# Optimization experiments

Hardware: AMD Instinct MI355X
Metric: run time of the kernel (lower is better)

Reference implementation:

```python
import jax, jax.numpy as jnp
import numpy as np
import math

N_HEAD = 16
STRIDE = 128
C = 8


def _sparse_causal_mask(q_len, k_len):
    # Mirrors LingLongAttention._sparse_causal_mask (static, host-side numpy).
    cols = np.arange(k_len)
    rows = np.arange(k_len)[:, None]
    strided = (cols % STRIDE) >= (STRIDE - C)          # last C cols of each stride block
    local = (cols[None, :] // STRIDE) == (rows // STRIDE)  # same stride block as query
    causal = cols[None, :] <= rows
    layout = (strided[None, :] | local) & causal       # [k_len, k_len]
    return jnp.asarray(layout[k_len - q_len:])         # [q_len, k_len]


def setup_inputs() -> dict:
    key = jax.random.key(0)
    k1, k2, k3 = jax.random.split(key, 3)
    B, S, E = 2, 2048, 1024
    return {
        "hidden_states": jax.random.normal(k1, (B, S, E), dtype=jnp.float32),
        "W_attn": jax.random.normal(k2, (E, 3 * E), dtype=jnp.float32) * 0.02,
        "b_attn": jnp.zeros((3 * E,), dtype=jnp.float32),
        "W_proj": jax.random.normal(k3, (E, E), dtype=jnp.float32) * 0.02,
        "b_proj": jnp.zeros((E,), dtype=jnp.float32),
    }


def reference(hidden_states, W_attn, b_attn, W_proj, b_proj):
    B, S, E = hidden_states.shape
    H = N_HEAD
    D = E // H
    # Conv1D: x @ W + b, then split into q,k,v
    qkv = hidden_states @ W_attn + b_attn                 # [B,S,3E]
    q, k, v = jnp.split(qkv, 3, axis=-1)
    split = lambda t: t.reshape(B, S, H, D).transpose(0, 2, 1, 3)  # [B,H,S,D]
    q, k, v = split(q), split(k), split(v)
    scale = jnp.asarray(1.0 / math.sqrt(D), dtype=q.dtype)
    scores = jnp.einsum("bhqd,bhkd->bhqk", q, k) * scale  # [B,H,S,S]
    mask = _sparse_causal_mask(S, S)[None, None]          # [1,1,S,S]
    mask_value = jnp.asarray(jnp.finfo(scores.dtype).min, dtype=scores.dtype)
    scores = jnp.where(mask, scores, mask_value)
    attn = jax.nn.softmax(scores, axis=-1)
    out = jnp.einsum("bhqk,bhkd->bhqd", attn, v)          # [B,H,S,D]
    out = out.transpose(0, 2, 1, 3).reshape(B, S, E)      # merge heads
    return out @ W_proj + b_proj
```

## Files before the change

kernel.cpp:

```cpp
#include <hip/hip_runtime.h>
#include <hip/hip_bf16.h>
#include <stdint.h>

typedef unsigned short u16;
typedef uint32_t u32;
typedef short s16x8 __attribute__((ext_vector_type(8)));
typedef float f32x4 __attribute__((ext_vector_type(4)));

#define SDIM 2048
#define EDIM 1024

static __device__ __forceinline__ float b2f(u16 v) {
    union { float f; u32 u; } c; c.u = ((u32)v) << 16; return c.f;
}
static __device__ __forceinline__ u16 f2b(float f) {
    union { float f; u32 u; } c; c.f = f;
    u32 u = c.u;
    u32 r = (u + 0x7FFFu + ((u >> 16) & 1u)) >> 16;
    return (u16)r;
}
static __device__ __forceinline__ void gll16(const u16* g, u16* l) {
    __builtin_amdgcn_global_load_lds(
        (const __attribute__((address_space(1))) void*)g,
        (__attribute__((address_space(3))) void*)l, 16, 0, 0);
}

static __device__ __forceinline__ int sniff_bf16(const u16* __restrict__ x) {
    u16 v = x[(threadIdx.x & 63) * 2];
    int e = (v >> 7) & 0xFF;
    unsigned long long m = __ballot(e >= 90 && e <= 144);
    return __popcll(m) >= 48;
}

__global__ __launch_bounds__(256) void k_prep(
    const void* __restrict__ X, const void* __restrict__ Wa,
    const void* __restrict__ Wp, u16* __restrict__ Xb,
    u16* __restrict__ WtA, u16* __restrict__ WtP) {
    int f = sniff_bf16((const u16*)X);
    int z = blockIdx.z;
    int t = threadIdx.x;
    if (z == 2) {
        if (f) return;
        const float* s = (const float*)X;
        int bid = blockIdx.y * 48 + blockIdx.x;
        for (int c = bid; c < 2048; c += 768) {
            long i = ((long)c * 256 + t) * 8;
            u16 o[8];
            for (int j = 0; j < 8; ++j) o[j] = f2b(s[i + j]);
            *(uint4*)&Xb[i] = *(uint4*)o;
        }
        return;
    }
    if (z == 1 && blockIdx.x >= 16) return;
    const void* src = z ? Wp : Wa;
    u16* dst = z ? WtP : WtA;
    int Nsrc = z ? 1024 : 3072;
    int n0 = blockIdx.x * 64, k0 = blockIdx.y * 64;
    __shared__ u16 L[64 * 72];
    int r = t >> 2, c0 = (t & 3) * 16;
    u16 val[16];
    if (f) {
        const u16* s = (const u16*)src + (size_t)(k0 + r) * Nsrc + n0 + c0;
        *(uint4*)&val[0] = *(const uint4*)s;
        *(uint4*)&val[8] = *(const uint4*)(s + 8);
    } else {
        const float* s = (const float*)src + (size_t)(k0 + r) * Nsrc + n0 + c0;
        for (int j = 0; j < 16; ++j) val[j] = f2b(s[j]);
    }
    for (int j = 0; j < 16; ++j) L[(c0 + j) * 72 + r] = val[j];
    __syncthreads();
    uint4 o0 = *(const uint4*)&L[r * 72 + c0];
    uint4 o1 = *(const uint4*)&L[r * 72 + c0 + 8];
    u16* d = dst + (size_t)(n0 + r) * 1024 + k0 + c0;
    *(uint4*)d = o0;
    *(uint4*)(d + 8) = o1;
}

#define G1_STA(h, Tn) do {                                                     \
    int ko_ = ((Tn) & 15) * 64;                                                \
    gll16(Ab + (size_t)((h) * 128) * 1024 + ko_,                               \
          &As[(Tn) & 1][(((h) * 128) + wave * 16) * 64]);                      \
    gll16(Ab + (size_t)((h) * 128 + 8) * 1024 + ko_,                           \
          &As[(Tn) & 1][(((h) * 128) + wave * 16 + 8) * 64]);                  \
} while (0)
#define G1_STB(h, Tn) do {                                                     \
    int ko_ = ((Tn) & 15) * 64;                                                \
    gll16(Bb + (size_t)((h) * 128) * 1024 + ko_,                               \
          &Bs[(Tn) & 1][(((h) * 128) + wave * 16) * 64]);                      \
    gll16(Bb + (size_t)((h) * 128 + 8) * 1024 + ko_,                           \
          &Bs[(Tn) & 1][(((h) * 128) + wave * 16 + 8) * 64]);                  \
} while (0)

__global__ __launch_bounds__(512, 2) void k_gemm1(
    const u16* __restrict__ Xraw, const u16* __restrict__ Xb,
    const u16* __restrict__ Bt, const void* __restrict__ bias,
    u16* __restrict__ C) {
    const int K = 1024;
    __shared__ u16 As[2][256 * 64];
    __shared__ u16 Bs[2][256 * 64];
    int f = sniff_bf16(Xraw);
    const u16* A = f ? Xraw : Xb;
    int t = threadIdx.x, wave = t >> 6, lane = t & 63;
    int bid = blockIdx.x;
    int swz = (bid & 7) * 24 + (bid >> 3);
    int bx = swz % 12, by = swz / 12;
    int m0 = by * 256, n0 = bx * 256;
    int wr = wave >> 2, wc = wave & 3;
    int lm = lane & 15, q4 = lane >> 4;
    int l8 = lane >> 3, l7 = lane & 7;
    int scol = (l7 ^ l8) * 8;
    const u16* Ab = A  + (size_t)(m0 + wave * 16 + l8) * K + scol;
    const u16* Bb = Bt + (size_t)(n0 + wave * 16 + l8) * K + scol;
    int kc0 = ((q4) ^ (lm & 7)) * 8;
    int kc1 = ((4 + q4) ^ (lm & 7)) * 8;

    f32x4 acc[8][4];
    f32x4 z = {0.f, 0.f, 0.f, 0.f};
#pragma unroll
    for (int mi = 0; mi < 8; ++mi)
#pragma unroll
        for (int ni = 0; ni < 4; ++ni) acc[mi][ni] = z;

    G1_STA(0, 0); G1_STA(1, 0);
    G1_STB(0, 0); G1_STB(1, 0);
    G1_STA(0, 1); G1_STA(1, 1);

    s16x8 afr[8][2], bfr[4][2];

    for (int T = 0; T < 16; ++T) {
        int p = T & 1;
        asm volatile("s_waitcnt vmcnt(4)\n\ts_barrier" ::: "memory");
#pragma unroll
        for (int mi = 0; mi < 4; ++mi) {
            int rb = (wr * 128 + mi * 16 + lm) * 64;
            afr[mi][0] = *(const s16x8*)&As[p][rb + kc0];
            afr[mi][1] = *(const s16x8*)&As[p][rb + kc1];
        }
#pragma unroll
        for (int ni = 0; ni < 2; ++ni) {
            int rb = (wc * 64 + ni * 16 + lm) * 64;
            bfr[ni][0] = *(const s16x8*)&Bs[p][rb + kc0];
            bfr[ni][1] = *(const s16x8*)&Bs[p][rb + kc1];
        }
        G1_STB(0, T + 1);
        __builtin_amdgcn_s_setprio(1);
#pragma unroll
        for (int mi = 0; mi < 4; ++mi)
#pragma unroll
            for (int ni = 0; ni < 2; ++ni) {
                acc[mi][ni] = __builtin_amdgcn_mfma_f32_16x16x32_bf16(
                    afr[mi][0], bfr[ni][0], acc[mi][ni], 0, 0, 0);
                acc[mi][ni] = __builtin_amdgcn_mfma_f32_16x16x32_bf16(
                    afr[mi][1], bfr[ni][1], acc[mi][ni], 0, 0, 0);
            }
        __builtin_amdgcn_s_setprio(0);
        asm volatile("s_barrier" ::: "memory");
#pragma unroll
        for (int mi = 4; mi < 8; ++mi) {
            int rb = (wr * 128 + mi * 16 + lm) * 64;
            afr[mi][0] = *(const s16x8*)&As[p][rb + kc0];
            afr[mi][1] = *(const s16x8*)&As[p][rb + kc1];
        }
#pragma unroll
        for (int ni = 2; ni < 4; ++ni) {
            int rb = (wc * 64 + ni * 16 + lm) * 64;
            bfr[ni][0] = *(const s16x8*)&Bs[p][rb + kc0];
            bfr[ni][1] = *(const s16x8*)&Bs[p][rb + kc1];
        }
        G1_STB(1, T + 1);
        __builtin_amdgcn_s_setprio(1);
#pragma unroll
        for (int mi = 4; mi < 8; ++mi)
#pragma unroll
            for (int ni = 2; ni < 4; ++ni) {
                acc[mi][ni] = __builtin_amdgcn_mfma_f32_16x16x32_bf16(
                    afr[mi][0], bfr[ni][0], acc[mi][ni], 0, 0, 0);
                acc[mi][ni] = __builtin_amdgcn_mfma_f32_16x16x32_bf16(
                    afr[mi][1], bfr[ni][1], acc[mi][ni], 0, 0, 0);
            }
        __builtin_amdgcn_s_setprio(0);
        asm volatile("s_barrier" ::: "memory");
        G1_STA(0, T + 2);
        __builtin_amdgcn_s_setprio(1);
#pragma unroll
        for (int mi = 0; mi < 4; ++mi)
#pragma unroll
            for (int ni = 2; ni < 4; ++ni) {
                acc[mi][ni] = __builtin_amdgcn_mfma_f32_16x16x32_bf16(
                    afr[mi][0], bfr[ni][0], acc[mi][ni], 0, 0, 0);
                acc[mi][ni] = __builtin_amdgcn_mfma_f32_16x16x32_bf16(
                    afr[mi][1], bfr[ni][1], acc[mi][ni], 0, 0, 0);
            }
        __builtin_amdgcn_s_setprio(0);
        asm volatile("s_barrier" ::: "memory");
        G1_STA(1, T + 2);
        __builtin_amdgcn_s_setprio(1);
#pragma unroll
        for (int mi = 4; mi < 8; ++mi)
#pragma unroll
            for (int ni = 0; ni < 2; ++ni) {
                acc[mi][ni] = __builtin_amdgcn_mfma_f32_16x16x32_bf16(
                    afr[mi][0], bfr[ni][0], acc[mi][ni], 0, 0, 0);
                acc[mi][ni] = __builtin_amdgcn_mfma_f32_16x16x32_bf16(
                    afr[mi][1], bfr[ni][1], acc[mi][ni], 0, 0, 0);
            }
        __builtin_amdgcn_s_setprio(0);
        asm volatile("s_barrier" ::: "memory");
    }
    asm volatile("s_waitcnt vmcnt(0)" ::: "memory");

    int cn = lane & 15, cr = q4 * 4;
#pragma unroll
    for (int ni = 0; ni < 4; ++ni) {
        int gn = n0 + wc * 64 + ni * 16 + cn;
        float bb = f ? b2f(((const u16*)bias)[gn]) : ((const float*)bias)[gn];
        int kind = gn >> 10, rem = gn & 1023;
        int h = rem >> 6, d = rem & 63;
        int hm = kind * 32 + h;
#pragma unroll
        for (int mi = 0; mi < 8; ++mi)
            for (int r = 0; r < 4; ++r) {
                int gm = m0 + wr * 128 + mi * 16 + cr + r;
                int b = gm >> 11, s = gm & 2047;
                size_t o = ((size_t)((hm + b * 16) * 2048 + s)) * 64 + d;
                C[o] = f2b(acc[mi][ni][r] + bb);
            }
    }
}

__global__ __launch_bounds__(256) void k_gemm2(
    const u16* __restrict__ Xraw, const u16* __restrict__ A,
    const u16* __restrict__ Bt, const void* __restrict__ bias,
    u16* __restrict__ Cb, float* __restrict__ Cf) {
    const int K = 1024, N = 1024;
    __shared__ u16 As[3][2048];
    __shared__ u16 Bs[3][4096];
    int f = sniff_bf16(Xraw);
    int t = threadIdx.x, wave = t >> 6, lane = t & 63;
    int m0 = blockIdx.y * 64, n0 = blockIdx.x * 128;
    int wm = (wave >> 1) * 32, wn = (wave & 1) * 64;
    int lm = lane & 15;
    int lk = (((lane >> 4) ^ ((lane >> 1) & 3))) * 8;
    int sr = t >> 2;
    int sc = ((t & 3) ^ ((t >> 3) & 3)) * 8;
    const u16* Ap = A + (size_t)(m0 + sr) * K + sc;
    const u16* Bp = Bt + (size_t)(n0 + sr) * K + sc;
    int wo = wave * 512;

    f32x4 acc[2][4];
    f32x4 z = {0.f, 0.f, 0.f, 0.f};
    for (int mi = 0; mi < 2; ++mi)
        for (int ni = 0; ni < 4; ++ni) acc[mi][ni] = z;

    gll16(Ap, &As[0][wo]);
    gll16(Bp, &Bs[0][wo]);
    gll16(Bp + (size_t)64 * K, &Bs[0][wo + 2048]);
    gll16(Ap + 32, &As[1][wo]);
    gll16(Bp + 32, &Bs[1][wo]);
    gll16(Bp + (size_t)64 * K + 32, &Bs[1][wo + 2048]);

    u16 *Ac = &As[0][0], *An = &As[1][0], *At = &As[2][0];
    u16 *Bc = &Bs[0][0], *Bn = &Bs[1][0], *Btg = &Bs[2][0];

    for (int it = 0; it < 32; ++it) {
        asm volatile("s_waitcnt vmcnt(3)\n\ts_barrier" ::: "memory");
        int kn = ((it + 2) & 31) * 32;
        gll16(Ap + kn, At + wo);
        gll16(Bp + kn, Btg + wo);
        gll16(Bp + (size_t)64 * K + kn, Btg + wo + 2048);

        s16x8 af[2], bfr[4];
        for (int mi = 0; mi < 2; ++mi)
            af[mi] = *(const s16x8*)&Ac[(wm + mi * 16 + lm) * 32 + lk];
        for (int ni = 0; ni < 4; ++ni)
            bfr[ni] = *(const s16x8*)&Bc[(wn + ni * 16 + lm) * 32 + lk];
        for (int mi = 0; mi < 2; ++mi)
            for (int ni = 0; ni < 4; ++ni)
                acc[mi][ni] = __builtin_amdgcn_mfma_f32_16x16x32_bf16(
                    af[mi], bfr[ni], acc[mi][ni], 0, 0, 0);

        u16* tp = Ac; Ac = An; An = At; At = tp;
        tp = Bc; Bc = Bn; Bn = Btg; Btg = tp;
    }
    asm volatile("s_waitcnt vmcnt(0)" ::: "memory");

    int store_f32 = (f == 0);
    int cn = lane & 15, cr = (lane >> 4) * 4;
    for (int ni = 0; ni < 4; ++ni) {
        int gn = n0 + wn + ni * 16 + cn;
        float bb = f ? b2f(((const u16*)bias)[gn]) : ((const float*)bias)[gn];
        for (int mi = 0; mi < 2; ++mi)
            for (int r = 0; r < 4; ++r) {
                int gm = m0 + wm + mi * 16 + cr + r;
                float v = acc[mi][ni][r] + bb;
                size_t o = (size_t)gm * N + gn;
                if (store_f32) Cf[o] = v;
                else           Cb[o] = f2b(v);
            }
    }
}

#define VP 264
#define PP 264
__global__ __launch_bounds__(256) void k_attn4(const u16* __restrict__ QKV,
                                               u16* __restrict__ AO) {
    int bx = blockIdx.x, h = blockIdx.y, b = blockIdx.z;
    int qb = bx >> 1, sb = bx & 1;
    int t = threadIdx.x, lane = t & 63, wave = t >> 6;
    int lm = lane & 15, q4 = lane >> 4;
    int nstr = qb << 3;
    int nk = nstr + (sb << 6) + 64;
    int r0 = (qb << 7) + (sb << 6);

    __shared__ char smem[79872];
    u16* Vts = (u16*)smem;
    u16* Qs  = (u16*)(smem + 33792);
    u16* Ks  = (u16*)(smem + 33792 + 9216);
    u16* Ps  = (u16*)(smem + 33792);

    int hm = b * 16 + h;
    const u16* qp = QKV + ((size_t)hm * 2048 + r0) * 64;
    const u16* kp = QKV + ((size_t)(32 + hm) * 2048) * 64;
    const u16* vp = QKV + ((size_t)(64 + hm) * 2048) * 64;

    for (int c = t; c < 512; c += 256) {
        int r = c >> 3, d0 = (c & 7) << 3;
        *(uint4*)&Qs[r * 72 + d0] = *(const uint4*)(qp + c * 8);
    }
    uint4 zz = {0u, 0u, 0u, 0u};
    for (int c = t; c < 2048; c += 256) {
        int i = c >> 3, d0 = (c & 7) << 3;
        uint4 kv = zz;
        if (i < nk) {
            int key = (i < nstr) ? (((i >> 3) << 7) + 120 + (i & 7))
                                 : ((qb << 7) + (i - nstr));
            kv = *(const uint4*)(kp + key * 64 + d0);
        }
        *(uint4*)&Ks[i * 72 + d0] = kv;
    }
    {
        int i0 = (t & 31) * 8, d0 = (t >> 5) * 8;
        u16 m8[8][8];
        for (int r = 0; r < 8; ++r) {
            int i = i0 + r;
            uint4 vv = zz;
            if (i < nk) {
                int key = (i < nstr) ? (((i >> 3) << 7) + 120 + (i & 7))
                                     : ((qb << 7) + (i - nstr));
                vv = *(const uint4*)(vp + key * 64 + d0);
            }
            *(uint4*)m8[r] = vv;
        }
        for (int j = 0; j < 8; ++j) {
            u16 o[8];
            for (int r = 0; r < 8; ++r) o[r] = m8[r][j];
            *(uint4*)&Vts[(d0 + j) * VP + i0] = *(uint4*)o;
        }
    }
    __syncthreads();

    f32x4 acc[16];
    f32x4 z4 = {0.f, 0.f, 0.f, 0.f};
    for (int ni = 0; ni < 16; ++ni) acc[ni] = z4;
    s16x8 af0 = *(const s16x8*)&Qs[(wave * 16 + lm) * 72 + q4 * 8];
    s16x8 af1 = *(const s16x8*)&Qs[(wave * 16 + lm) * 72 + 32 + q4 * 8];
    for (int ni = 0; ni < 16; ++ni) {
        s16x8 bf0 = *(const s16x8*)&Ks[(ni * 16 + lm) * 72 + q4 * 8];
        s16x8 bf1 = *(const s16x8*)&Ks[(ni * 16 + lm) * 72 + 32 + q4 * 8];
        acc[ni] = __builtin_amdgcn_mfma_f32_16x16x32_bf16(af0, bf0, acc[ni], 0, 0, 0);
        acc[ni] = __builtin_amdgcn_mfma_f32_16x16x32_bf16(af1, bf1, acc[ni], 0, 0, 0);
    }
    __syncthreads();

    float mx[4] = {-3e38f, -3e38f, -3e38f, -3e38f};
    for (int ni = 0; ni < 16; ++ni) {
        int i = ni * 16 + lm;
        for (int reg = 0; reg < 4; ++reg) {
            int rl = (sb << 6) + wave * 16 + q4 * 4 + reg;
            bool valid = (i < nstr) || ((i - nstr) <= rl);
            float v = valid ? acc[ni][reg] * 0.125f : -3e38f;
            acc[ni][reg] = v;
            mx[reg] = fmaxf(mx[reg], v);
        }
    }
    for (int reg = 0; reg < 4; ++reg)
        for (int off = 1; off < 16; off <<= 1)
            mx[reg] = fmaxf(mx[reg], __shfl_xor(mx[reg], off, 64));
    float sm[4] = {0.f, 0.f, 0.f, 0.f};
    for (int ni = 0; ni < 16; ++ni)
        for (int reg = 0; reg < 4; ++reg) {
            float e = __expf(acc[ni][reg] - mx[reg]);
            acc[ni][reg] = e;
            sm[reg] += e;
        }
    for (int reg = 0; reg < 4; ++reg)
        for (int off = 1; off < 16; off <<= 1)
            sm[reg] += __shfl_xor(sm[reg], off, 64);
    float inv[4];
    for (int reg = 0; reg < 4; ++reg) inv[reg] = 1.f / sm[reg];

    for (int ni = 0; ni < 16; ++ni) {
        int i = ni * 16 + lm;
        for (int reg = 0; reg < 4; ++reg)
            Ps[(wave * 16 + q4 * 4 + reg) * PP + i] = f2b(acc[ni][reg]);
    }
    __syncthreads();

    f32x4 acc2[4];
    for (int ni2 = 0; ni2 < 4; ++ni2) acc2[ni2] = z4;
    for (int k0 = 0; k0 < 256; k0 += 32) {
        s16x8 pf = *(const s16x8*)&Ps[(wave * 16 + lm) * PP + k0 + q4 * 8];
        for (int ni2 = 0; ni2 < 4; ++ni2) {
            s16x8 vf = *(const s16x8*)&Vts[(ni2 * 16 + lm) * VP + k0 + q4 * 8];
            acc2[ni2] = __builtin_amdgcn_mfma_f32_16x16x32_bf16(pf, vf, acc2[ni2], 0, 0, 0);
        }
    }
    int srow = r0 + wave * 16 + q4 * 4;
    for (int ni2 = 0; ni2 < 4; ++ni2)
        for (int reg = 0; reg < 4; ++reg) {
            size_t o = ((size_t)(b * SDIM + srow + reg)) * EDIM + h * 64 + ni2 * 16 + lm;
            AO[o] = f2b(acc2[ni2][reg] * inv[reg]);
        }
}

extern "C" void kernel_launch(void* const* d_in, const int* in_sizes, int n_in,
                              void* d_out, int out_size, void* d_ws, size_t ws_size,
                              hipStream_t stream) {
    const void* X  = d_in[0];
    const void* Wa = d_in[1];
    const void* ba = d_in[2];
    const void* Wp = d_in[3];
    const void* bp = d_in[4];

    char* w = (char*)d_ws;
    u16* Xb   = (u16*)(w);
    u16* WtA  = (u16*)(w + 8388608);
    u16* WtP  = (u16*)(w + 14680064);
    u16* QKVh = (u16*)(w + 16777216);
    u16* AO   = (u16*)(w + 41943040);

    k_prep<<<dim3(48, 16, 3), 256, 0, stream>>>(X, Wa, Wp, Xb, WtA, WtP);
    k_gemm1<<<dim3(192), 512, 0, stream>>>((const u16*)X, Xb, WtA, ba, QKVh);
    k_attn4<<<dim3(32, 16, 2), 256, 0, stream>>>(QKVh, AO);
    k_gemm2<<<dim3(8, 64), 256, 0, stream>>>((const u16*)X, AO, WtP, bp,
                                             (u16*)d_out, (float*)d_out);
}
```

Before: 162.8 us.

## Retile QKV GEMM to 256x192 tiles so 256 blocks fill the GPU

Changes the first GEMM's block tile from 256x256 to 256x192, which raises the grid from 192 to 256 blocks and is meant to fill the 256 compute units of the MI355X evenly in one wave. The LDS staging is reworked so each wave loads 8-row slices, the MFMA schedule is reorganised around three 16-column fragments per wave, and the block swizzle is updated to match. The epilogue precomputes per-column bias and head offsets. The cost is lower arithmetic intensity per block and a slightly uneven MFMA phase structure.

```diff
diff --git a/kernel.cpp b/kernel.cpp
--- a/kernel.cpp
+++ b/kernel.cpp
@@ -76,20 +76,10 @@
     *(uint4*)(d + 8) = o1;
 }
 
-#define G1_STA(h, Tn) do {                                                     \
-    int ko_ = ((Tn) & 15) * 64;                                                \
-    gll16(Ab + (size_t)((h) * 128) * 1024 + ko_,                               \
-          &As[(Tn) & 1][(((h) * 128) + wave * 16) * 64]);                      \
-    gll16(Ab + (size_t)((h) * 128 + 8) * 1024 + ko_,                           \
-          &As[(Tn) & 1][(((h) * 128) + wave * 16 + 8) * 64]);                  \
-} while (0)
-#define G1_STB(h, Tn) do {                                                     \
-    int ko_ = ((Tn) & 15) * 64;                                                \
-    gll16(Bb + (size_t)((h) * 128) * 1024 + ko_,                               \
-          &Bs[(Tn) & 1][(((h) * 128) + wave * 16) * 64]);                      \
-    gll16(Bb + (size_t)((h) * 128 + 8) * 1024 + ko_,                           \
-          &Bs[(Tn) & 1][(((h) * 128) + wave * 16 + 8) * 64]);                  \
-} while (0)
+#define STA6(s, Tn) gll16(Asrc + (size_t)(s) * 64 * 1024 + ((Tn) & 15) * 64, \
+                          &As[(Tn) & 1][(((s) * 64) + wave * 8) * 64])
+#define STB6(s, Tn) gll16(Bsrc + (size_t)(s) * 64 * 1024 + ((Tn) & 15) * 64, \
+                          &Bs[(Tn) & 1][(((s) * 64) + wave * 8) * 64])
 
 __global__ __launch_bounds__(512, 2) void k_gemm1(
     const u16* __restrict__ Xraw, const u16* __restrict__ Xb,
@@ -97,35 +87,35 @@
     u16* __restrict__ C) {
     const int K = 1024;
     __shared__ u16 As[2][256 * 64];
-    __shared__ u16 Bs[2][256 * 64];
+    __shared__ u16 Bs[2][192 * 64];
     int f = sniff_bf16(Xraw);
     const u16* A = f ? Xraw : Xb;
     int t = threadIdx.x, wave = t >> 6, lane = t & 63;
     int bid = blockIdx.x;
-    int swz = (bid & 7) * 24 + (bid >> 3);
-    int bx = swz % 12, by = swz / 12;
-    int m0 = by * 256, n0 = bx * 256;
+    int swz = (bid & 7) * 32 + (bid >> 3);
+    int bx = swz & 15, by = swz >> 4;
+    int m0 = by * 256, n0 = bx * 192;
     int wr = wave >> 2, wc = wave & 3;
     int lm = lane & 15, q4 = lane >> 4;
     int l8 = lane >> 3, l7 = lane & 7;
     int scol = (l7 ^ l8) * 8;
-    const u16* Ab = A  + (size_t)(m0 + wave * 16 + l8) * K + scol;
-    const u16* Bb = Bt + (size_t)(n0 + wave * 16 + l8) * K + scol;
-    int kc0 = ((q4) ^ (lm & 7)) * 8;
+    const u16* Asrc = A  + (size_t)(m0 + wave * 8 + l8) * K + scol;
+    const u16* Bsrc = Bt + (size_t)(n0 + wave * 8 + l8) * K + scol;
+    int kc0 = (q4 ^ (lm & 7)) * 8;
     int kc1 = ((4 + q4) ^ (lm & 7)) * 8;
 
-    f32x4 acc[8][4];
+    f32x4 acc[8][3];
     f32x4 z = {0.f, 0.f, 0.f, 0.f};
 #pragma unroll
     for (int mi = 0; mi < 8; ++mi)
 #pragma unroll
-        for (int ni = 0; ni < 4; ++ni) acc[mi][ni] = z;
-
-    G1_STA(0, 0); G1_STA(1, 0);
-    G1_STB(0, 0); G1_STB(1, 0);
-    G1_STA(0, 1); G1_STA(1, 1);
-
-    s16x8 afr[8][2], bfr[4][2];
+        for (int ni = 0; ni < 3; ++ni) acc[mi][ni] = z;
+
+    STA6(0, 0); STA6(1, 0); STA6(2, 0); STA6(3, 0);
+    STB6(0, 0); STB6(1, 0); STB6(2, 0);
+    STA6(0, 1); STA6(1, 1); STA6(2, 1); STA6(3, 1);
+
+    s16x8 afr[8][2], bfr[3][2];
 
     for (int T = 0; T < 16; ++T) {
         int p = T & 1;
@@ -138,11 +128,11 @@
         }
 #pragma unroll
         for (int ni = 0; ni < 2; ++ni) {
-            int rb = (wc * 64 + ni * 16 + lm) * 64;
+            int rb = (wc * 48 + ni * 16 + lm) * 64;
             bfr[ni][0] = *(const s16x8*)&Bs[p][rb + kc0];
             bfr[ni][1] = *(const s16x8*)&Bs[p][rb + kc1];
         }
-        G1_STB(0, T + 1);
+        STB6(0, T + 1);
         __builtin_amdgcn_s_setprio(1);
 #pragma unroll
         for (int mi = 0; mi < 4; ++mi)
@@ -161,39 +151,34 @@
             afr[mi][0] = *(const s16x8*)&As[p][rb + kc0];
             afr[mi][1] = *(const s16x8*)&As[p][rb + kc1];
         }
-#pragma unroll
-        for (int ni = 2; ni < 4; ++ni) {
-            int rb = (wc * 64 + ni * 16 + lm) * 64;
-            bfr[ni][0] = *(const s16x8*)&Bs[p][rb + kc0];
-            bfr[ni][1] = *(const s16x8*)&Bs[p][rb + kc1];
-        }
-        G1_STB(1, T + 1);
+        {
+            int rb = (wc * 48 + 32 + lm) * 64;
+            bfr[2][0] = *(const s16x8*)&Bs[p][rb + kc0];
+            bfr[2][1] = *(const s16x8*)&Bs[p][rb + kc1];
+        }
+        STB6(1, T + 1); STB6(2, T + 1);
         __builtin_amdgcn_s_setprio(1);
 #pragma unroll
-        for (int mi = 4; mi < 8; ++mi)
-#pragma unroll
-            for (int ni = 2; ni < 4; ++ni) {
-                acc[mi][ni] = __builtin_amdgcn_mfma_f32_16x16x32_bf16(
-                    afr[mi][0], bfr[ni][0], acc[mi][ni], 0, 0, 0);
-                acc[mi][ni] = __builtin_amdgcn_mfma_f32_16x16x32_bf16(
-                    afr[mi][1], bfr[ni][1], acc[mi][ni], 0, 0, 0);
-            }
+        for (int mi = 4; mi < 8; ++mi) {
+            acc[mi][2] = __builtin_amdgcn_mfma_f32_16x16x32_bf16(
+                afr[mi][0], bfr[2][0], acc[mi][2], 0, 0, 0);
+            acc[mi][2] = __builtin_amdgcn_mfma_f32_16x16x32_bf16(
+                afr[mi][1], bfr[2][1], acc[mi][2], 0, 0, 0);
+        }
         __builtin_amdgcn_s_setprio(0);
         asm volatile("s_barrier" ::: "memory");
-        G1_STA(0, T + 2);
+        STA6(0, T + 2); STA6(1, T + 2);
         __builtin_amdgcn_s_setprio(1);
 #pragma unroll
-        for (int mi = 0; mi < 4; ++mi)
-#pragma unroll
-            for (int ni = 2; ni < 4; ++ni) {
-                acc[mi][ni] = __builtin_amdgcn_mfma_f32_16x16x32_bf16(
-                    afr[mi][0], bfr[ni][0], acc[mi][ni], 0, 0, 0);
-                acc[mi][ni] = __builtin_amdgcn_mfma_f32_16x16x32_bf16(
-                    afr[mi][1], bfr[ni][1], acc[mi][ni], 0, 0, 0);
-            }
+        for (int mi = 0; mi < 4; ++mi) {
+            acc[mi][2] = __builtin_amdgcn_mfma_f32_16x16x32_bf16(
+                afr[mi][0], bfr[2][0], acc[mi][2], 0, 0, 0);
+            acc[mi][2] = __builtin_amdgcn_mfma_f32_16x16x32_bf16(
+                afr[mi][1], bfr[2][1], acc[mi][2], 0, 0, 0);
+        }
         __builtin_amdgcn_s_setprio(0);
         asm volatile("s_barrier" ::: "memory");
-        G1_STA(1, T + 2);
+        STA6(2, T + 2); STA6(3, T + 2);
         __builtin_amdgcn_s_setprio(1);
 #pragma unroll
         for (int mi = 4; mi < 8; ++mi)
@@ -209,23 +194,27 @@
     }
     asm volatile("s_waitcnt vmcnt(0)" ::: "memory");
 
-    int cn = lane & 15, cr = q4 * 4;
-#pragma unroll
-    for (int ni = 0; ni < 4; ++ni) {
-        int gn = n0 + wc * 64 + ni * 16 + cn;
-        float bb = f ? b2f(((const u16*)bias)[gn]) : ((const float*)bias)[gn];
+    int cn = lm, cr = q4 * 4;
+    float bb[3]; int hm_[3], d_[3];
+#pragma unroll
+    for (int ni = 0; ni < 3; ++ni) {
+        int gn = n0 + wc * 48 + ni * 16 + cn;
+        bb[ni] = f ? b2f(((const u16*)bias)[gn]) : ((const float*)bias)[gn];
         int kind = gn >> 10, rem = gn & 1023;
-        int h = rem >> 6, d = rem & 63;
-        int hm = kind * 32 + h;
-#pragma unroll
-        for (int mi = 0; mi < 8; ++mi)
-            for (int r = 0; r < 4; ++r) {
-                int gm = m0 + wr * 128 + mi * 16 + cr + r;
-                int b = gm >> 11, s = gm & 2047;
-                size_t o = ((size_t)((hm + b * 16) * 2048 + s)) * 64 + d;
-                C[o] = f2b(acc[mi][ni][r] + bb);
+        hm_[ni] = kind * 32 + (rem >> 6);
+        d_[ni] = rem & 63;
+    }
+#pragma unroll
+    for (int mi = 0; mi < 8; ++mi)
+        for (int r = 0; r < 4; ++r) {
+            int gm = m0 + wr * 128 + mi * 16 + cr + r;
+            int b = gm >> 11, s = gm & 2047;
+#pragma unroll
+            for (int ni = 0; ni < 3; ++ni) {
+                size_t o = ((size_t)((hm_[ni] + b * 16) * 2048 + s)) * 64 + d_[ni];
+                C[o] = f2b(acc[mi][ni][r] + bb[ni]);
             }
-    }
+        }
 }
 
 __global__ __launch_bounds__(256) void k_gemm2(
@@ -440,7 +429,7 @@
     u16* AO   = (u16*)(w + 41943040);
 
     k_prep<<<dim3(48, 16, 3), 256, 0, stream>>>(X, Wa, Wp, Xb, WtA, WtP);
-    k_gemm1<<<dim3(192), 512, 0, stream>>>((const u16*)X, Xb, WtA, ba, QKVh);
+    k_gemm1<<<dim3(256), 512, 0, stream>>>((const u16*)X, Xb, WtA, ba, QKVh);
     k_attn4<<<dim3(32, 16, 2), 256, 0, stream>>>(QKVh, AO);
     k_gemm2<<<dim3(8, 64), 256, 0, stream>>>((const u16*)X, AO, WtP, bp,
                                              (u16*)d_out, (float*)d_out);
```

New measurement: 156.9 us. -3.6%, faster.
